# Performance work log

Hardware: AMD Instinct MI355X
Metric: run time of the kernel (lower is better)

The kernel has to match this reference:

```python
import jax, jax.numpy as jnp
import numpy as np

B, S, D = 2, 1024, 1024
E, K, I = 8, 2, 1024
LIMIT = 7.0
ALPHA = 1.702


def setup_inputs() -> dict:
    key = jax.random.key(0)
    k0, k1, k2, k3 = jax.random.split(key, 4)
    return {
        "x": jax.random.normal(k0, (B, S, D), jnp.float32),
        "norm_w": jnp.ones((D,), jnp.float32),
        "gate_w": jax.random.normal(k1, (E, D), jnp.float32) / np.sqrt(D).astype(np.float32),
        "gate_b": jnp.zeros((E,), jnp.float32),
        "mlp1_w": jax.random.normal(k2, (E, 2 * I, D), jnp.float32) / np.sqrt(D).astype(np.float32),
        "mlp1_b": jnp.zeros((E, 2 * I), jnp.float32),
        "mlp2_w": jax.random.normal(k3, (E, D, I), jnp.float32) / np.sqrt(I).astype(np.float32),
        "mlp2_b": jnp.zeros((E, D), jnp.float32),
    }


def _swiglu(t, limit):
    # interleaved gate/linear split (gpt-oss style) with clamping
    glu = jnp.minimum(t[..., ::2], limit)
    lin = jnp.clip(t[..., 1::2], -limit, limit)
    return glu * jax.nn.sigmoid(ALPHA * glu) * (lin + 1.0)


def reference(x, norm_w, gate_w, gate_b, mlp1_w, mlp1_b, mlp2_w, mlp2_b):
    eps = jnp.finfo(x.dtype).eps
    # RMSNorm
    h = x * jax.lax.rsqrt(jnp.mean(x * x, axis=-1, keepdims=True) + eps) * norm_w
    flat = h.reshape(-1, D)                              # [T, D]
    # top-k gating
    logits = flat @ gate_w.T + gate_b                    # [T, E]
    vals, idx = jax.lax.top_k(logits, K)                 # sorted descending
    wts = jax.nn.softmax(vals, axis=-1)                  # [T, K]
    # per-expert SwiGLU MLP (dense over experts, identical math to per-token gather)
    t1 = jnp.einsum('td,efd->tef', flat, mlp1_w) + mlp1_b   # [T, E, 2I]
    act = _swiglu(t1, LIMIT)                                 # [T, E, I]
    y = jnp.einsum('tei,edi->ted', act, mlp2_w) + mlp2_b     # [T, E, D]
    # gather selected experts and combine
    sel = jnp.take_along_axis(y, idx[:, :, None], axis=1)    # [T, K, D]
    out = jnp.sum(sel * wts[:, :, None], axis=1).reshape(x.shape)
    return x + out
```

## Files before the change

### kernel.cpp

```cpp
#include <hip/hip_runtime.h>
#include <stdint.h>

#define TNUM 2048
#define DDIM 1024
#define NEXP 8
#define KSEL 2
#define IDIM 1024
#define TWOI 2048
#define LIMITV 7.0f
#define ALPHAV 1.702f
#define ROWT_MAX 40
#define RMSB (TNUM / 4)
#define N81 (NEXP * TWOI * DDIM / 8)
#define N82 (NEXP * DDIM * IDIM / 8)
#define G1TOT (ROWT_MAX * (TWOI / 128))
#define G2TOT (2 * ROWT_MAX * (DDIM / 128))

typedef __attribute__((ext_vector_type(8))) short bf16x8;
typedef __attribute__((ext_vector_type(4))) float f32x4;

#define VMCNT8() asm volatile("s_waitcnt vmcnt(8)" ::: "memory")
#define VMCNT0() asm volatile("s_waitcnt vmcnt(0)" ::: "memory")
#define BARRIER() asm volatile("s_barrier" ::: "memory")

__device__ __forceinline__ unsigned short f2bf(float f) {
  unsigned u = __float_as_uint(f);
  u += 0x7FFF + ((u >> 16) & 1);
  return (unsigned short)(u >> 16);
}

__device__ __forceinline__ int4 cvt8(float4 a, float4 b) {
  union { unsigned short us[8]; int4 v; } o;
  o.us[0] = f2bf(a.x); o.us[1] = f2bf(a.y); o.us[2] = f2bf(a.z); o.us[3] = f2bf(a.w);
  o.us[4] = f2bf(b.x); o.us[5] = f2bf(b.y); o.us[6] = f2bf(b.z); o.us[7] = f2bf(b.w);
  return o.v;
}

__device__ __forceinline__ float4 ld4bf(const unsigned short* p) {
  int2 v = *(const int2*)p;
  unsigned a = (unsigned)v.x, b = (unsigned)v.y;
  float4 r;
  r.x = __uint_as_float((a & 0xFFFFu) << 16);
  r.y = __uint_as_float(a & 0xFFFF0000u);
  r.z = __uint_as_float((b & 0xFFFFu) << 16);
  r.w = __uint_as_float(b & 0xFFFF0000u);
  return r;
}

__device__ __forceinline__ void gl2lds16(const void* g, void* l) {
  __builtin_amdgcn_global_load_lds(
      (__attribute__((address_space(1))) unsigned int*)(uintptr_t)g,
      (__attribute__((address_space(3))) unsigned int*)(uintptr_t)l, 16, 0, 0);
}

__device__ __forceinline__ int xcd_swz(int bid, int total) {
  int q = total >> 3, r = total & 7;
  int xcd = bid & 7, pos = bid >> 3;
  return (xcd < r ? xcd * (q + 1) : r * (q + 1) + (xcd - r) * q) + pos;
}

__global__ __launch_bounds__(256) void k_rms_cvt(
    const float* __restrict__ x, const float* __restrict__ norm_w,
    const float* __restrict__ gate_w, const float* __restrict__ gate_b,
    const float* __restrict__ w1f, unsigned short* __restrict__ w1b,
    unsigned short* __restrict__ hb, int* __restrict__ tidx,
    float* __restrict__ twt) {
  if ((int)blockIdx.x >= RMSB) {
    int k0 = ((int)blockIdx.x - RMSB) * 1024 + (int)threadIdx.x;
    const float4* s = (const float4*)w1f;
#pragma unroll
    for (int i = 0; i < 4; ++i) {
      int k = k0 + i * 256;
      if (k < N81) ((int4*)w1b)[k] = cvt8(s[2 * k], s[2 * k + 1]);
    }
    return;
  }
  const int lane = threadIdx.x & 63;
  const int t = blockIdx.x * 4 + (threadIdx.x >> 6);

  const float4* xr  = (const float4*)x + (size_t)t * 256 + lane * 4;
  const float4* nwr = (const float4*)norm_w + lane * 4;
  const float4* gbr = (const float4*)gate_b;
  float4 xv[4], nwv[4];
#pragma unroll
  for (int i = 0; i < 4; ++i) xv[i] = xr[i];
  float4 gb0 = gbr[0], gb1 = gbr[1];
#pragma unroll
  for (int i = 0; i < 4; ++i) nwv[i] = nwr[i];

  float ss = 0.f;
#pragma unroll
  for (int i = 0; i < 4; ++i)
    ss += xv[i].x * xv[i].x + xv[i].y * xv[i].y + xv[i].z * xv[i].z + xv[i].w * xv[i].w;
#pragma unroll
  for (int m = 1; m < 64; m <<= 1) ss += __shfl_xor(ss, m);
  const float sc = rsqrtf(ss * (1.0f / DDIM) + 1.1920929e-07f);

  float4 h[4];
#pragma unroll
  for (int i = 0; i < 4; ++i) {
    h[i].x = xv[i].x * sc * nwv[i].x;
    h[i].y = xv[i].y * sc * nwv[i].y;
    h[i].z = xv[i].z * sc * nwv[i].z;
    h[i].w = xv[i].w * sc * nwv[i].w;
  }
  int4* hw = (int4*)(hb + (size_t)t * DDIM + lane * 16);
  hw[0] = cvt8(h[0], h[1]);
  hw[1] = cvt8(h[2], h[3]);

  float p[NEXP];
#pragma unroll
  for (int e = 0; e < NEXP; ++e) {
    const float4* g4 = (const float4*)gate_w + e * 256 + lane * 4;
    float4 a = g4[0], b = g4[1], c = g4[2], d = g4[3];
    p[e] = h[0].x * a.x + h[0].y * a.y + h[0].z * a.z + h[0].w * a.w
         + h[1].x * b.x + h[1].y * b.y + h[1].z * b.z + h[1].w * b.w
         + h[2].x * c.x + h[2].y * c.y + h[2].z * c.z + h[2].w * c.w
         + h[3].x * d.x + h[3].y * d.y + h[3].z * d.z + h[3].w * d.w;
  }
#pragma unroll
  for (int m = 1; m < 64; m <<= 1) {
#pragma unroll
    for (int e = 0; e < NEXP; ++e) p[e] += __shfl_xor(p[e], m);
  }
  p[0] += gb0.x; p[1] += gb0.y; p[2] += gb0.z; p[3] += gb0.w;
  p[4] += gb1.x; p[5] += gb1.y; p[6] += gb1.z; p[7] += gb1.w;

  if (lane == 0) {
    int i0 = 0; float v0 = p[0];
#pragma unroll
    for (int e = 1; e < NEXP; ++e) if (p[e] > v0) { v0 = p[e]; i0 = e; }
    int i1 = -1; float v1 = -3.4e38f;
#pragma unroll
    for (int e = 0; e < NEXP; ++e) if (e != i0 && p[e] > v1) { v1 = p[e]; i1 = e; }
    float e1 = __expf(v1 - v0);
    float w0 = 1.f / (1.f + e1);
    int2 ip; ip.x = i0; ip.y = i1;
    float2 wp; wp.x = w0; wp.y = e1 * w0;
    ((int2*)tidx)[t] = ip;
    ((float2*)twt)[t] = wp;
  }
}

__global__ __launch_bounds__(512) void k_sched(
    const int* __restrict__ tidx, int* __restrict__ meta,
    int* __restrict__ tl, int* __restrict__ rows, int* __restrict__ sof) {
  __shared__ unsigned short cnt[256][NEXP];
  __shared__ int off[NEXP];
  __shared__ int tot[NEXP];
  const int tid = threadIdx.x;
  int e_[16], rel_[16];
  if (tid < 256) {
#pragma unroll
    for (int k = 0; k < 16; ++k) e_[k] = tidx[tid * 16 + k];
#pragma unroll
    for (int k = 0; k < 16; ++k) {
      int r = 0;
#pragma unroll
      for (int j2 = 0; j2 < 16; ++j2)
        if (j2 < k) r += (e_[j2] == e_[k]) ? 1 : 0;
      rel_[k] = r;
    }
#pragma unroll
    for (int e = 0; e < NEXP; ++e) {
      int c = 0;
#pragma unroll
      for (int k = 0; k < 16; ++k) c += (e_[k] == e) ? 1 : 0;
      cnt[tid][e] = (unsigned short)c;
    }
  }
  __syncthreads();
  {
    const int we = tid >> 6, lane = tid & 63;
    int carry = 0;
#pragma unroll
    for (int chunk = 0; chunk < 4; ++chunk) {
      int i = chunk * 64 + lane;
      int c = (int)cnt[i][we];
      int s = c;
#pragma unroll
      for (int o = 1; o < 64; o <<= 1) {
        int t2 = __shfl_up(s, o);
        if (lane >= o) s += t2;
      }
      cnt[i][we] = (unsigned short)(s - c + carry);
      carry += __shfl(s, 63);
    }
    if (lane == 0) tot[we] = carry;
  }
  __syncthreads();
  if (tid == 0) {
    int acc = 0, nt = 0;
    for (int e = 0; e < NEXP; ++e) {
      meta[8 + e] = acc; off[e] = acc;
      int c = tot[e]; acc += c;
      int ntile = (c + 127) >> 7;
      for (int r = 0; r < ntile; ++r) tl[nt++] = (e << 8) | r;
    }
    meta[16] = acc;
    meta[25] = nt;
  }
  __syncthreads();
  if (tid < 256) {
#pragma unroll
    for (int k = 0; k < 16; ++k) {
      int i = tid * 16 + k;
      int e = e_[k];
      int slot = off[e] + (int)cnt[tid][e] + rel_[k];
      rows[slot] = i >> 1;
      sof[i] = slot;
    }
  }
}

__global__ __launch_bounds__(256, 2) void k_gemm1(
    const unsigned short* __restrict__ hb, const unsigned short* __restrict__ w1b,
    const float* __restrict__ mlp1_b, const int* __restrict__ meta,
    const int* __restrict__ tl, const int* __restrict__ rows,
    const float* __restrict__ w2f, unsigned short* __restrict__ w2b,
    unsigned short* __restrict__ actb) {
  const int bid = blockIdx.x;
  const int tid = threadIdx.x, lane = tid & 63, wid = tid >> 6;
  if (bid >= G1TOT) {
    int k0 = (bid - G1TOT) * 1024 + tid;
    const float4* s = (const float4*)w2f;
#pragma unroll
    for (int i = 0; i < 4; ++i) {
      int k = k0 + i * 256;
      if (k < N82) ((int4*)w2b)[k] = cvt8(s[2 * k], s[2 * k + 1]);
    }
    return;
  }
  const int nt = meta[25];
  const int total = nt * (TWOI / 128);
  if (bid >= total) return;
  const int j = xcd_swz(bid, total);
  const int ct = j / nt;
  const int tile = tl[j - ct * nt];
  const int e = tile >> 8, rt = tile & 255;
  const int offs = meta[8 + e];
  const int n_e = meta[9 + e] - offs;

  __shared__ unsigned short As[2][128][64];
  __shared__ unsigned short Bs[2][128][64];
  __shared__ int srow[128];
  if (tid < 128) srow[tid] = rows[offs + min(rt * 128 + tid, n_e - 1)];
  __syncthreads();

  const int rloc = tid >> 3;
  const int csw  = (((tid & 7) ^ (rloc & 7)) << 3);
  const unsigned short* gA[4];
  const unsigned short* gB[4];
  const unsigned short* w1e = w1b + (size_t)e * TWOI * DDIM;
#pragma unroll
  for (int jj = 0; jj < 4; ++jj) {
    gA[jj] = hb + (size_t)srow[jj * 32 + rloc] * DDIM + csw;
    gB[jj] = w1e + (size_t)(ct * 128 + jj * 32 + rloc) * DDIM + csw;
  }

#define G1_STAGE(BUF, KT)                                                      \
  _Pragma("unroll") for (int jj = 0; jj < 4; ++jj) {                           \
    gl2lds16(gA[jj] + (KT) * 64, &As[BUF][0][0] + jj * 2048 + tid * 8);        \
    gl2lds16(gB[jj] + (KT) * 64, &Bs[BUF][0][0] + jj * 2048 + tid * 8);        \
  }

  f32x4 acc[4][4];
#pragma unroll
  for (int m = 0; m < 4; ++m)
#pragma unroll
    for (int n = 0; n < 4; ++n) acc[m][n] = (f32x4){0.f, 0.f, 0.f, 0.f};

  const int wr = wid >> 1, wc = wid & 1;
  const int lrow = lane & 15, ksub = (lane >> 4) * 8;
  const int NK = DDIM / 64;

  G1_STAGE(0, 0)
#pragma unroll
  for (int kt = 0; kt < NK; ++kt) {
    const int cur = kt & 1;
    if (kt + 1 < NK) {
      G1_STAGE(cur ^ 1, kt + 1)
      VMCNT8();
    } else {
      VMCNT0();
    }
    BARRIER();
#pragma unroll
    for (int kk = 0; kk < 2; ++kk) {
      bf16x8 af[4], bfr[4];
#pragma unroll
      for (int m = 0; m < 4; ++m) {
        int row = wr * 64 + m * 16 + lrow;
        int chunk = ((kk * 32 + ksub) >> 3) ^ (row & 7);
        af[m] = *(const bf16x8*)&As[cur][row][chunk * 8];
      }
#pragma unroll
      for (int n = 0; n < 4; ++n) {
        int row = wc * 64 + n * 16 + lrow;
        int chunk = ((kk * 32 + ksub) >> 3) ^ (row & 7);
        bfr[n] = *(const bf16x8*)&Bs[cur][row][chunk * 8];
      }
#pragma unroll
      for (int m = 0; m < 4; ++m)
#pragma unroll
        for (int n = 0; n < 4; ++n)
          acc[m][n] = __builtin_amdgcn_mfma_f32_16x16x32_bf16(af[m], bfr[n], acc[m][n], 0, 0, 0);
    }
    BARRIER();
  }
#undef G1_STAGE

  const float* b1e = mlp1_b + e * TWOI;
#pragma unroll
  for (int m = 0; m < 4; ++m) {
#pragma unroll
    for (int n = 0; n < 4; ++n) {
      int cg = ct * 128 + wc * 64 + n * 16 + (lane & 15);
      float bias = b1e[cg];
#pragma unroll
      for (int j2 = 0; j2 < 4; ++j2) {
        float val = acc[m][n][j2] + bias;
        float part = __shfl_xor(val, 1);
        int rl = wr * 64 + m * 16 + ((lane >> 4) << 2) + j2;
        if (!(lane & 1)) {
          float glu = fminf(val, LIMITV);
          float lin = fminf(fmaxf(part, -LIMITV), LIMITV);
          float s = 1.f / (1.f + __expf(-ALPHAV * glu));
          float a = glu * s * (lin + 1.f);
          if (rt * 128 + rl < n_e)
            actb[(size_t)(offs + rt * 128 + rl) * IDIM + (cg >> 1)] = f2bf(a);
        }
      }
    }
  }
}

__global__ __launch_bounds__(256, 2) void k_gemm2(
    const unsigned short* __restrict__ actb, const unsigned short* __restrict__ w2b,
    const float* __restrict__ mlp2_b, const int* __restrict__ meta,
    const int* __restrict__ tl, unsigned short* __restrict__ ybuf) {
  const int nt = meta[25];
  const int totalK = nt * (DDIM / 128) * 2;
  const int bid = blockIdx.x;
  if (bid >= totalK) return;
  const int j = xcd_swz(bid, totalK);
  const int kp = j & 1;
  const int jt = j >> 1;
  const int ct = jt / nt;
  const int tile = tl[jt - ct * nt];
  const int e = tile >> 8, rt = tile & 255;
  const int offs = meta[8 + e];
  const int n_e = meta[9 + e] - offs;
  const int tid = threadIdx.x, lane = tid & 63, wid = tid >> 6;

  __shared__ unsigned short As[2][128][64];
  __shared__ unsigned short Bs[2][128][64];

  const int rloc = tid >> 3;
  const int csw  = (((tid & 7) ^ (rloc & 7)) << 3);
  const int koff = kp * 512;
  const unsigned short* gA[4];
  const unsigned short* gB[4];
  const unsigned short* w2e = w2b + (size_t)e * DDIM * IDIM;
#pragma unroll
  for (int jj = 0; jj < 4; ++jj) {
    gA[jj] = actb + (size_t)(offs + min(rt * 128 + jj * 32 + rloc, n_e - 1)) * IDIM + koff + csw;
    gB[jj] = w2e + (size_t)(ct * 128 + jj * 32 + rloc) * IDIM + koff + csw;
  }

#define G2_STAGE(BUF, KT)                                                      \
  _Pragma("unroll") for (int jj = 0; jj < 4; ++jj) {                           \
    gl2lds16(gA[jj] + (KT) * 64, &As[BUF][0][0] + jj * 2048 + tid * 8);        \
    gl2lds16(gB[jj] + (KT) * 64, &Bs[BUF][0][0] + jj * 2048 + tid * 8);        \
  }

  f32x4 acc[4][4];
#pragma unroll
  for (int m = 0; m < 4; ++m)
#pragma unroll
    for (int n = 0; n < 4; ++n) acc[m][n] = (f32x4){0.f, 0.f, 0.f, 0.f};

  const int wr = wid >> 1, wc = wid & 1;
  const int lrow = lane & 15, ksub = (lane >> 4) * 8;
  const int NK = 512 / 64;

  G2_STAGE(0, 0)
#pragma unroll
  for (int kt = 0; kt < NK; ++kt) {
    const int cur = kt & 1;
    if (kt + 1 < NK) {
      G2_STAGE(cur ^ 1, kt + 1)
      VMCNT8();
    } else {
      VMCNT0();
    }
    BARRIER();
#pragma unroll
    for (int kk = 0; kk < 2; ++kk) {
      bf16x8 af[4], bfr[4];
#pragma unroll
      for (int m = 0; m < 4; ++m) {
        int row = wr * 64 + m * 16 + lrow;
        int chunk = ((kk * 32 + ksub) >> 3) ^ (row & 7);
        af[m] = *(const bf16x8*)&As[cur][row][chunk * 8];
      }
#pragma unroll
      for (int n = 0; n < 4; ++n) {
        int row = wc * 64 + n * 16 + lrow;
        int chunk = ((kk * 32 + ksub) >> 3) ^ (row & 7);
        bfr[n] = *(const bf16x8*)&Bs[cur][row][chunk * 8];
      }
#pragma unroll
      for (int m = 0; m < 4; ++m)
#pragma unroll
        for (int n = 0; n < 4; ++n)
          acc[m][n] = __builtin_amdgcn_mfma_f32_16x16x32_bf16(af[m], bfr[n], acc[m][n], 0, 0, 0);
    }
    BARRIER();
  }
#undef G2_STAGE

  const float* b2e = mlp2_b + e * DDIM;
  unsigned short* yh = ybuf + (size_t)kp * TNUM * KSEL * DDIM;
#pragma unroll
  for (int m = 0; m < 4; ++m) {
#pragma unroll
    for (int n = 0; n < 4; ++n) {
      int d = ct * 128 + wc * 64 + n * 16 + (lane & 15);
      float bias = kp ? 0.f : b2e[d];
#pragma unroll
      for (int j2 = 0; j2 < 4; ++j2) {
        int rl = wr * 64 + m * 16 + ((lane >> 4) << 2) + j2;
        if (rt * 128 + rl < n_e)
          yh[(size_t)(offs + rt * 128 + rl) * DDIM + d] = f2bf(acc[m][n][j2] + bias);
      }
    }
  }
}

__global__ __launch_bounds__(256) void k_combine(
    const float* __restrict__ x, const unsigned short* __restrict__ ybuf,
    const int* __restrict__ sof, const float* __restrict__ twt,
    float* __restrict__ out) {
  int t = blockIdx.x, tid = threadIdx.x;
  int s0 = sof[2 * t], s1 = sof[2 * t + 1];
  float w0 = twt[2 * t], w1 = twt[2 * t + 1];
  const size_t H = (size_t)TNUM * KSEL * DDIM;
  float4 xv = ((const float4*)x)[t * 256 + tid];
  float4 a0 = ld4bf(ybuf + (size_t)s0 * DDIM + tid * 4);
  float4 a1 = ld4bf(ybuf + H + (size_t)s0 * DDIM + tid * 4);
  float4 b0 = ld4bf(ybuf + (size_t)s1 * DDIM + tid * 4);
  float4 b1 = ld4bf(ybuf + H + (size_t)s1 * DDIM + tid * 4);
  float4 o;
  o.x = xv.x + w0 * (a0.x + a1.x) + w1 * (b0.x + b1.x);
  o.y = xv.y + w0 * (a0.y + a1.y) + w1 * (b0.y + b1.y);
  o.z = xv.z + w0 * (a0.z + a1.z) + w1 * (b0.z + b1.z);
  o.w = xv.w + w0 * (a0.w + a1.w) + w1 * (b0.w + b1.w);
  ((float4*)out)[t * 256 + tid] = o;
}

extern "C" void kernel_launch(void* const* d_in, const int* in_sizes, int n_in,
                              void* d_out, int out_size, void* d_ws, size_t ws_size,
                              hipStream_t stream) {
  const float* x      = (const float*)d_in[0];
  const float* norm_w = (const float*)d_in[1];
  const float* gate_w = (const float*)d_in[2];
  const float* gate_b = (const float*)d_in[3];
  const float* mlp1_w = (const float*)d_in[4];
  const float* mlp1_b = (const float*)d_in[5];
  const float* mlp2_w = (const float*)d_in[6];
  const float* mlp2_b = (const float*)d_in[7];
  float* out = (float*)d_out;

  char* w = (char*)d_ws;
  unsigned short* w1b = (unsigned short*)w; w += (size_t)NEXP * TWOI * DDIM * 2;
  unsigned short* w2b = (unsigned short*)w; w += (size_t)NEXP * DDIM * IDIM * 2;
  unsigned short* hb  = (unsigned short*)w; w += (size_t)TNUM * DDIM * 2;
  unsigned short* actb = (unsigned short*)w; w += (size_t)TNUM * KSEL * IDIM * 2;
  unsigned short* ybuf = (unsigned short*)w; w += (size_t)2 * TNUM * KSEL * DDIM * 2;
  int*   tidx = (int*)w;  w += TNUM * KSEL * 4;
  float* twt  = (float*)w; w += TNUM * KSEL * 4;
  int*   sof  = (int*)w;  w += TNUM * KSEL * 4;
  int*   rows = (int*)w;  w += TNUM * KSEL * 4;
  int*   meta = (int*)w;  w += 32 * 4;
  int*   tl   = (int*)w;  w += 64 * 4;

  k_rms_cvt<<<RMSB + N81 / 1024, 256, 0, stream>>>(x, norm_w, gate_w, gate_b,
                                                   mlp1_w, w1b, hb, tidx, twt);
  k_sched<<<1, 512, 0, stream>>>(tidx, meta, tl, rows, sof);
  k_gemm1<<<G1TOT + N82 / 1024, 256, 0, stream>>>(hb, w1b, mlp1_b, meta, tl, rows,
                                                  mlp2_w, w2b, actb);
  k_gemm2<<<G2TOT, 256, 0, stream>>>(actb, w2b, mlp2_b, meta, tl, ybuf);
  k_combine<<<TNUM, 256, 0, stream>>>(x, ybuf, sof, twt, out);
}
```

Baseline: 109.8 us.

## Replace double-buffered LDS pipeline with single buffer and raise occupancy to 4

Both expert GEMM kernels drop the two-stage LDS double buffer and load each K tile synchronously into one buffer, then wait on all loads and a barrier before the MFMA work. This halves shared memory per block, and launch bounds go from 2 to 4 blocks per CU, so latency is meant to be hidden by other resident blocks instead of in-block prefetch. The trade-off is no load/compute overlap within a block, plus register pressure from the tighter launch bound that could cause spills.

```diff
diff --git a/kernel.cpp b/kernel.cpp
--- a/kernel.cpp
+++ b/kernel.cpp
@@ -19,7 +19,6 @@
 typedef __attribute__((ext_vector_type(8))) short bf16x8;
 typedef __attribute__((ext_vector_type(4))) float f32x4;
 
-#define VMCNT8() asm volatile("s_waitcnt vmcnt(8)" ::: "memory")
 #define VMCNT0() asm volatile("s_waitcnt vmcnt(0)" ::: "memory")
 #define BARRIER() asm volatile("s_barrier" ::: "memory")
 
@@ -213,7 +212,7 @@
   }
 }
 
-__global__ __launch_bounds__(256, 2) void k_gemm1(
+__global__ __launch_bounds__(256, 4) void k_gemm1(
     const unsigned short* __restrict__ hb, const unsigned short* __restrict__ w1b,
     const float* __restrict__ mlp1_b, const int* __restrict__ meta,
     const int* __restrict__ tl, const int* __restrict__ rows,
@@ -241,8 +240,8 @@
   const int offs = meta[8 + e];
   const int n_e = meta[9 + e] - offs;
 
-  __shared__ unsigned short As[2][128][64];
-  __shared__ unsigned short Bs[2][128][64];
+  __shared__ unsigned short As[128][64];
+  __shared__ unsigned short Bs[128][64];
   __shared__ int srow[128];
   if (tid < 128) srow[tid] = rows[offs + min(rt * 128 + tid, n_e - 1)];
   __syncthreads();
@@ -258,10 +257,10 @@
     gB[jj] = w1e + (size_t)(ct * 128 + jj * 32 + rloc) * DDIM + csw;
   }
 
-#define G1_STAGE(BUF, KT)                                                      \
+#define G1_STAGE(KT)                                                           \
   _Pragma("unroll") for (int jj = 0; jj < 4; ++jj) {                           \
-    gl2lds16(gA[jj] + (KT) * 64, &As[BUF][0][0] + jj * 2048 + tid * 8);        \
-    gl2lds16(gB[jj] + (KT) * 64, &Bs[BUF][0][0] + jj * 2048 + tid * 8);        \
+    gl2lds16(gA[jj] + (KT) * 64, &As[0][0] + jj * 2048 + tid * 8);             \
+    gl2lds16(gB[jj] + (KT) * 64, &Bs[0][0] + jj * 2048 + tid * 8);             \
   }
 
   f32x4 acc[4][4];
@@ -274,16 +273,10 @@
   const int lrow = lane & 15, ksub = (lane >> 4) * 8;
   const int NK = DDIM / 64;
 
-  G1_STAGE(0, 0)
 #pragma unroll
   for (int kt = 0; kt < NK; ++kt) {
-    const int cur = kt & 1;
-    if (kt + 1 < NK) {
-      G1_STAGE(cur ^ 1, kt + 1)
-      VMCNT8();
-    } else {
-      VMCNT0();
-    }
+    G1_STAGE(kt)
+    VMCNT0();
     BARRIER();
 #pragma unroll
     for (int kk = 0; kk < 2; ++kk) {
@@ -292,13 +285,13 @@
       for (int m = 0; m < 4; ++m) {
         int row = wr * 64 + m * 16 + lrow;
         int chunk = ((kk * 32 + ksub) >> 3) ^ (row & 7);
-        af[m] = *(const bf16x8*)&As[cur][row][chunk * 8];
+        af[m] = *(const bf16x8*)&As[row][chunk * 8];
       }
 #pragma unroll
       for (int n = 0; n < 4; ++n) {
         int row = wc * 64 + n * 16 + lrow;
         int chunk = ((kk * 32 + ksub) >> 3) ^ (row & 7);
-        bfr[n] = *(const bf16x8*)&Bs[cur][row][chunk * 8];
+        bfr[n] = *(const bf16x8*)&Bs[row][chunk * 8];
       }
 #pragma unroll
       for (int m = 0; m < 4; ++m)
@@ -335,7 +328,7 @@
   }
 }
 
-__global__ __launch_bounds__(256, 2) void k_gemm2(
+__global__ __launch_bounds__(256, 4) void k_gemm2(
     const unsigned short* __restrict__ actb, const unsigned short* __restrict__ w2b,
     const float* __restrict__ mlp2_b, const int* __restrict__ meta,
     const int* __restrict__ tl, unsigned short* __restrict__ ybuf) {
@@ -353,8 +346,8 @@
   const int n_e = meta[9 + e] - offs;
   const int tid = threadIdx.x, lane = tid & 63, wid = tid >> 6;
 
-  __shared__ unsigned short As[2][128][64];
-  __shared__ unsigned short Bs[2][128][64];
+  __shared__ unsigned short As[128][64];
+  __shared__ unsigned short Bs[128][64];
 
   const int rloc = tid >> 3;
   const int csw  = (((tid & 7) ^ (rloc & 7)) << 3);
@@ -368,10 +361,10 @@
     gB[jj] = w2e + (size_t)(ct * 128 + jj * 32 + rloc) * IDIM + koff + csw;
   }
 
-#define G2_STAGE(BUF, KT)                                                      \
+#define G2_STAGE(KT)                                                           \
   _Pragma("unroll") for (int jj = 0; jj < 4; ++jj) {                           \
-    gl2lds16(gA[jj] + (KT) * 64, &As[BUF][0][0] + jj * 2048 + tid * 8);        \
-    gl2lds16(gB[jj] + (KT) * 64, &Bs[BUF][0][0] + jj * 2048 + tid * 8);        \
+    gl2lds16(gA[jj] + (KT) * 64, &As[0][0] + jj * 2048 + tid * 8);             \
+    gl2lds16(gB[jj] + (KT) * 64, &Bs[0][0] + jj * 2048 + tid * 8);             \
   }
 
   f32x4 acc[4][4];
@@ -384,16 +377,10 @@
   const int lrow = lane & 15, ksub = (lane >> 4) * 8;
   const int NK = 512 / 64;
 
-  G2_STAGE(0, 0)
 #pragma unroll
   for (int kt = 0; kt < NK; ++kt) {
-    const int cur = kt & 1;
-    if (kt + 1 < NK) {
-      G2_STAGE(cur ^ 1, kt + 1)
-      VMCNT8();
-    } else {
-      VMCNT0();
-    }
+    G2_STAGE(kt)
+    VMCNT0();
     BARRIER();
 #pragma unroll
     for (int kk = 0; kk < 2; ++kk) {
@@ -402,13 +389,13 @@
       for (int m = 0; m < 4; ++m) {
         int row = wr * 64 + m * 16 + lrow;
         int chunk = ((kk * 32 + ksub) >> 3) ^ (row & 7);
-        af[m] = *(const bf16x8*)&As[cur][row][chunk * 8];
+        af[m] = *(const bf16x8*)&As[row][chunk * 8];
       }
 #pragma unroll
       for (int n = 0; n < 4; ++n) {
         int row = wc * 64 + n * 16 + lrow;
         int chunk = ((kk * 32 + ksub) >> 3) ^ (row & 7);
-        bfr[n] = *(const bf16x8*)&Bs[cur][row][chunk * 8];
+        bfr[n] = *(const bf16x8*)&Bs[row][chunk * 8];
       }
 #pragma unroll
       for (int m = 0; m < 4; ++m)
```

Measured after the change: 100.3 us (median of 3 runs). -8.6%, faster.
